# Kernel optimization log

Measured on AMD Instinct MI355X. Metric: run time of the kernel, lower is better.

Reference implementation:

```python
import jax, jax.numpy as jnp
import numpy as np

N = 50000      # nodes
E = 800000     # edges (avg degree 16)
D = 128        # node_embedding_dim
H = 256        # hidden_dim


def setup_inputs() -> dict:
    key = jax.random.key(0)
    ks = jax.random.split(key, 12)
    init = lambda k, shape, fan: (jax.random.normal(k, shape, jnp.float32) / np.sqrt(fan).astype(np.float32))
    return {
        "node_ids": jnp.arange(N, dtype=jnp.int32),
        "edge_index": jax.random.randint(ks[0], (2, E), 0, N, jnp.int32),
        "neighbour_edge_index": jax.random.randint(ks[1], (2, E), 0, N, jnp.int32),
        "edge_attr": jax.random.uniform(ks[2], (E,), jnp.float32),
        "emb": init(ks[3], (N, D), D),          # Embedding table
        "W_in": init(ks[4], (D, H), D), "b_in": jnp.zeros((H,), jnp.float32),
        "W_out": init(ks[5], (H, D), H), "b_out": jnp.zeros((D,), jnp.float32),
        "W1": init(ks[6], (2 * D, D), 2 * D), "b1": jnp.zeros((D,), jnp.float32),
        "W2": init(ks[7], (D, D), D), "b2": jnp.zeros((D,), jnp.float32),
        "W3": init(ks[8], (D, 1), D), "b3": jnp.zeros((1,), jnp.float32),
    }


def gcn_conv(x, W, b, edge_index, w):
    """PyG GCNConv, add_self_loops=False, normalize=True.
    out_i = b + sum_{(j->i)} d_i^{-1/2} w_ji d_j^{-1/2} (x_j @ W)
    deg_i = sum of incoming edge weights at target node i.
    """
    row, col = edge_index[0], edge_index[1]
    deg = jax.ops.segment_sum(w, col, num_segments=N)
    dinv = jnp.where(deg > 0, 1.0 / jnp.sqrt(deg), 0.0)
    norm = dinv[row] * w * dinv[col]                    # [E]
    h = x @ W                                           # [N, out]
    msg = h[row] * norm[:, None]                        # [E, out]
    return jax.ops.segment_sum(msg, col, num_segments=N) + b


def reference(node_ids, edge_index, neighbour_edge_index, edge_attr,
              emb, W_in, b_in, W_out, b_out, W1, b1, W2, b2, W3, b3):
    x = emb[node_ids]                                   # embedding lookup [N, D]
    x = jax.nn.elu(gcn_conv(x, W_in, b_in, edge_index, edge_attr))
    ones = jnp.ones((neighbour_edge_index.shape[1],), x.dtype)
    x = jax.nn.elu(gcn_conv(x, W_out, b_out, neighbour_edge_index, ones))
    # edge-level gather-concat-MLP decoder
    src, dst = edge_index[0], edge_index[1]
    h = jnp.concatenate([x[src], x[dst]], axis=1)       # [E, 2D]
    h = jax.nn.relu(h @ W1 + b1)
    h = jax.nn.relu(h @ W2 + b2)
    return (h @ W3 + b3).squeeze(-1)                    # [E]
```

## Files before the change

### kernel.cpp

```cpp
#include <hip/hip_runtime.h>
#include <math.h>

#define NN 50000
#define NE 800000

typedef __attribute__((ext_vector_type(8))) short s8_t;
typedef __attribute__((ext_vector_type(4))) float f4_t;

__device__ __forceinline__ short bf16_rne(float v) {
  unsigned u = __float_as_uint(v);
  unsigned r = (u + 0x7FFFu + ((u >> 16) & 1u)) >> 16;
  return (short)r;
}
__device__ __forceinline__ float bf16_tof(short h) {
  return __uint_as_float(((unsigned)(unsigned short)h) << 16);
}
__device__ __forceinline__ void split2(float v, short& hi, short& lo) {
  hi = bf16_rne(v);
  lo = bf16_rne(v - bf16_tof(hi));
}


__global__ __launch_bounds__(256) void k_wcvt(const float* __restrict__ W1,
                                              const float* __restrict__ W2,
                                              short* __restrict__ w1th,
                                              short* __restrict__ w1tl,
                                              short* __restrict__ w2th,
                                              short* __restrict__ w2tl) {
  int i = blockIdx.x * 256 + threadIdx.x;
  if (i < 32768) {
    int k = i >> 7, n = i & 127;
    short h, l; split2(W1[i], h, l);
    w1th[n * 256 + k] = h; w1tl[n * 256 + k] = l;
  } else if (i < 49152) {
    int j = i - 32768;
    int k = j >> 7, n = j & 127;
    short h, l; split2(W2[j], h, l);
    w2th[n * 128 + k] = h; w2tl[n * 128 + k] = l;
  }
}


__global__ __launch_bounds__(256) void k_hist(const int* __restrict__ ei,
                                              const int* __restrict__ nei,
                                              const float* __restrict__ w,
                                              int* __restrict__ cnt1,
                                              float* __restrict__ deg1,
                                              int* __restrict__ cnt2) {
  int e = blockIdx.x * 256 + threadIdx.x;
  if (e < NE) {
    int c1 = ei[NE + e];
    atomicAdd(&cnt1[c1], 1);
    atomicAdd(&deg1[c1], w[e]);
    atomicAdd(&cnt2[nei[NE + e]], 1);
  }
}

__global__ __launch_bounds__(256) void k_dinvs(const float* __restrict__ deg1,
                                               const int* __restrict__ cnt2,
                                               float* __restrict__ dinv1,
                                               float* __restrict__ dinv2) {
  int i = blockIdx.x * 256 + threadIdx.x;
  if (i < NN) {
    float d1 = deg1[i];
    dinv1[i] = d1 > 0.f ? (1.0f / sqrtf(d1)) : 0.f;
    int c2 = cnt2[i];
    dinv2[i] = c2 > 0 ? (1.0f / sqrtf((float)c2)) : 0.f;
  }
}


#define NCHUNK 196

__global__ __launch_bounds__(256) void k_scan_part(const int* __restrict__ cnt1,
                                                   const int* __restrict__ cnt2,
                                                   int* __restrict__ part) {
  int g = blockIdx.x >= NCHUNK;
  int chunk = g ? blockIdx.x - NCHUNK : blockIdx.x;
  const int* cnt = g ? cnt2 : cnt1;
  int i = chunk * 256 + threadIdx.x;
  int v = (i < NN) ? cnt[i] : 0;
  __shared__ int sd[4];
#pragma unroll
  for (int o = 32; o; o >>= 1) v += __shfl_down(v, o);
  if ((threadIdx.x & 63) == 0) sd[threadIdx.x >> 6] = v;
  __syncthreads();
  if (threadIdx.x == 0) part[blockIdx.x] = sd[0] + sd[1] + sd[2] + sd[3];
}

__global__ __launch_bounds__(256) void k_scan_mid(int* __restrict__ part,
                                                  int* __restrict__ off1_last,
                                                  int* __restrict__ off2_last) {
  __shared__ int sd[256];
  for (int g = 0; g < 2; g++) {
    int base = g * NCHUNK;
    int v = (threadIdx.x < NCHUNK) ? part[base + threadIdx.x] : 0;
    sd[threadIdx.x] = v;
    __syncthreads();
    for (int o = 1; o < 256; o <<= 1) {
      int x = (threadIdx.x >= o) ? sd[threadIdx.x - o] : 0;
      __syncthreads();
      sd[threadIdx.x] += x;
      __syncthreads();
    }
    if (threadIdx.x < NCHUNK) part[base + threadIdx.x] = sd[threadIdx.x] - v;
    if (threadIdx.x == 255) *(g ? off2_last : off1_last) = sd[255];
    __syncthreads();
  }
}

__global__ __launch_bounds__(256) void k_scan_final(const int* __restrict__ cnt1,
                                                    const int* __restrict__ cnt2,
                                                    const int* __restrict__ part,
                                                    int* __restrict__ off1,
                                                    int* __restrict__ pos1,
                                                    int* __restrict__ off2,
                                                    int* __restrict__ pos2) {
  int g = blockIdx.x >= NCHUNK;
  int chunk = g ? blockIdx.x - NCHUNK : blockIdx.x;
  const int* cnt = g ? cnt2 : cnt1;
  int* off = g ? off2 : off1;
  int* pos = g ? pos2 : pos1;
  __shared__ int sd[256];
  int i = chunk * 256 + threadIdx.x;
  int v = (i < NN) ? cnt[i] : 0;
  sd[threadIdx.x] = v;
  __syncthreads();
  for (int o = 1; o < 256; o <<= 1) {
    int x = (threadIdx.x >= o) ? sd[threadIdx.x - o] : 0;
    __syncthreads();
    sd[threadIdx.x] += x;
    __syncthreads();
  }
  if (i < NN) {
    int ex = part[blockIdx.x] + sd[threadIdx.x] - v;
    off[i] = ex; pos[i] = ex;
  }
}


__global__ __launch_bounds__(256) void k_fill(const int* __restrict__ ei,
                                              const int* __restrict__ nei,
                                              const float* __restrict__ w,
                                              const float* __restrict__ dinv1,
                                              const float* __restrict__ dinv2,
                                              int* __restrict__ pos1,
                                              int4* __restrict__ c1pack,
                                              int* __restrict__ pos2,
                                              int2* __restrict__ c2pack) {
  int e = blockIdx.x * 256 + threadIdx.x;
  if (e < NE) {
    int r = ei[e], c = ei[NE + e];
    float nv = dinv1[r] * w[e] * dinv1[c];
    int s = atomicAdd(&pos1[c], 1);
    c1pack[s] = make_int4(r, c, e, __float_as_int(nv));
    int r2 = nei[e], c2v = nei[NE + e];
    float nv2 = dinv2[r2] * dinv2[c2v];
    int s2 = atomicAdd(&pos2[c2v], 1);
    c2pack[s2] = make_int2(r2, __float_as_int(nv2));
  }
}


__global__ __launch_bounds__(256) void k_agg1(const int* __restrict__ off,
                                              const int4* __restrict__ c1pack,
                                              const int* __restrict__ ids,
                                              const float* __restrict__ emb,
                                              float* __restrict__ aggX) {
  int wave = threadIdx.x >> 6, lane = threadIdx.x & 63;
  int node = blockIdx.x * 4 + wave;
  int start = off[node], end = off[node + 1];
  float2 acc = make_float2(0.f, 0.f);
  int i = start;
  for (; i + 7 < end; i += 8) {
    float2 v[8]; float n[8];
#pragma unroll
    for (int k = 0; k < 8; k++) {
      int4 p = c1pack[i + k];
      n[k] = __int_as_float(p.w);
      v[k] = *(const float2*)(emb + (size_t)ids[p.x] * 128 + lane * 2);
    }
#pragma unroll
    for (int k = 0; k < 8; k++) {
      acc.x = fmaf(n[k], v[k].x, acc.x);
      acc.y = fmaf(n[k], v[k].y, acc.y);
    }
  }
  for (; i < end; i++) {
    int4 p = c1pack[i];
    float n0 = __int_as_float(p.w);
    float2 v0 = *(const float2*)(emb + (size_t)ids[p.x] * 128 + lane * 2);
    acc.x = fmaf(n0, v0.x, acc.x);
    acc.y = fmaf(n0, v0.y, acc.y);
  }
  *(float2*)(aggX + (size_t)node * 128 + lane * 2) = acc;
}


__global__ __launch_bounds__(256) void k_agg2(const int* __restrict__ off,
                                              const int2* __restrict__ c2pack,
                                              const float* __restrict__ h2,
                                              const float* __restrict__ b,
                                              short* __restrict__ xh,
                                              short* __restrict__ xl) {
  int wave = threadIdx.x >> 6, lane = threadIdx.x & 63;
  int node = blockIdx.x * 4 + wave;
  int start = off[node], end = off[node + 1];
  float2 acc = make_float2(0.f, 0.f);
  int i = start;
  for (; i + 7 < end; i += 8) {
    float2 v[8]; float n[8];
#pragma unroll
    for (int k = 0; k < 8; k++) {
      int2 p = c2pack[i + k];
      n[k] = __int_as_float(p.y);
      v[k] = *(const float2*)(h2 + (size_t)p.x * 128 + lane * 2);
    }
#pragma unroll
    for (int k = 0; k < 8; k++) {
      acc.x = fmaf(n[k], v[k].x, acc.x);
      acc.y = fmaf(n[k], v[k].y, acc.y);
    }
  }
  for (; i < end; i++) {
    int2 p = c2pack[i];
    float n0 = __int_as_float(p.y);
    float2 v0 = *(const float2*)(h2 + (size_t)p.x * 128 + lane * 2);
    acc.x = fmaf(n0, v0.x, acc.x);
    acc.y = fmaf(n0, v0.y, acc.y);
  }
  float vx = acc.x + b[lane * 2];
  float vy = acc.y + b[lane * 2 + 1];
  vx = vx > 0.f ? vx : expm1f(vx);
  vy = vy > 0.f ? vy : expm1f(vy);
  short hx, lx, hy, ly;
  split2(vx, hx, lx);
  split2(vy, hy, ly);
  unsigned hp = (unsigned)(unsigned short)hx | ((unsigned)(unsigned short)hy << 16);
  unsigned lp = (unsigned)(unsigned short)lx | ((unsigned)(unsigned short)ly << 16);
  *(unsigned*)(xh + (size_t)node * 128 + lane * 2) = hp;
  *(unsigned*)(xl + (size_t)node * 128 + lane * 2) = lp;
}


__global__ __launch_bounds__(256) void k_gemm_aggin(const float* __restrict__ X,
                                                    const float* __restrict__ W,
                                                    const float* __restrict__ b,
                                                    float* __restrict__ C) {
  __shared__ float As[32][128];
  int r0 = blockIdx.x * 32;
  int t = threadIdx.x;
  for (int i = t; i < 1024; i += 256) {
    int r = i >> 5, q = (i & 31) << 2;
    int rr = r0 + r;
    float4 v = make_float4(0.f, 0.f, 0.f, 0.f);
    if (rr < NN) v = *(const float4*)(X + (size_t)rr * 128 + q);
    *(float4*)(&As[r][q]) = v;
  }
  __syncthreads();
  int tc = t & 31, tr = t >> 5;
  int c0 = tc * 8, rr0 = tr * 4;
  float acc[4][8];
#pragma unroll
  for (int r = 0; r < 4; r++)
#pragma unroll
    for (int c = 0; c < 8; c++) acc[r][c] = 0.f;

  for (int k0 = 0; k0 < 128; k0 += 4) {
    float a_[4][4];
#pragma unroll
    for (int r = 0; r < 4; r++) {
      float4 v = *(const float4*)(&As[rr0 + r][k0]);
      a_[r][0] = v.x; a_[r][1] = v.y; a_[r][2] = v.z; a_[r][3] = v.w;
    }
#pragma unroll
    for (int kk = 0; kk < 4; kk++) {
      float4 w0 = *(const float4*)(W + (size_t)(k0 + kk) * 256 + c0);
      float4 w1 = *(const float4*)(W + (size_t)(k0 + kk) * 256 + c0 + 4);
#pragma unroll
      for (int r = 0; r < 4; r++) {
        float av = a_[r][kk];
        acc[r][0] += av * w0.x; acc[r][1] += av * w0.y;
        acc[r][2] += av * w0.z; acc[r][3] += av * w0.w;
        acc[r][4] += av * w1.x; acc[r][5] += av * w1.y;
        acc[r][6] += av * w1.z; acc[r][7] += av * w1.w;
      }
    }
  }
  float4 bb0 = *(const float4*)(b + c0);
  float4 bb1 = *(const float4*)(b + c0 + 4);
#pragma unroll
  for (int r = 0; r < 4; r++) {
    int rr = r0 + rr0 + r;
    if (rr < NN) {
      float o[8];
      o[0] = acc[r][0] + bb0.x; o[1] = acc[r][1] + bb0.y;
      o[2] = acc[r][2] + bb0.z; o[3] = acc[r][3] + bb0.w;
      o[4] = acc[r][4] + bb1.x; o[5] = acc[r][5] + bb1.y;
      o[6] = acc[r][6] + bb1.z; o[7] = acc[r][7] + bb1.w;
#pragma unroll
      for (int c = 0; c < 8; c++) o[c] = o[c] > 0.f ? o[c] : expm1f(o[c]);
      *(float4*)(C + (size_t)rr * 256 + c0) = make_float4(o[0], o[1], o[2], o[3]);
      *(float4*)(C + (size_t)rr * 256 + c0 + 4) = make_float4(o[4], o[5], o[6], o[7]);
    }
  }
}


__global__ __launch_bounds__(256) void k_gemm_mid(const float* __restrict__ X,
                                                  const float* __restrict__ W,
                                                  float* __restrict__ C) {
  __shared__ float As[32][256];
  int r0 = blockIdx.x * 32;
  int t = threadIdx.x;
  for (int i = t; i < 2048; i += 256) {
    int r = i >> 6, q = (i & 63) << 2;
    int rr = r0 + r;
    float4 v = make_float4(0.f, 0.f, 0.f, 0.f);
    if (rr < NN) v = *(const float4*)(X + (size_t)rr * 256 + q);
    *(float4*)(&As[r][q]) = v;
  }
  __syncthreads();
  int tc = t & 31, tr = t >> 5;
  int c0 = tc * 4, rr0 = tr * 4;
  float acc[4][4];
#pragma unroll
  for (int r = 0; r < 4; r++)
#pragma unroll
    for (int c = 0; c < 4; c++) acc[r][c] = 0.f;

  for (int k0 = 0; k0 < 256; k0 += 4) {
    float a_[4][4];
#pragma unroll
    for (int r = 0; r < 4; r++) {
      float4 v = *(const float4*)(&As[rr0 + r][k0]);
      a_[r][0] = v.x; a_[r][1] = v.y; a_[r][2] = v.z; a_[r][3] = v.w;
    }
#pragma unroll
    for (int kk = 0; kk < 4; kk++) {
      float4 w = *(const float4*)(W + (size_t)(k0 + kk) * 128 + c0);
#pragma unroll
      for (int r = 0; r < 4; r++) {
        float av = a_[r][kk];
        acc[r][0] += av * w.x; acc[r][1] += av * w.y;
        acc[r][2] += av * w.z; acc[r][3] += av * w.w;
      }
    }
  }
#pragma unroll
  for (int r = 0; r < 4; r++) {
    int rr = r0 + rr0 + r;
    if (rr < NN) {
      float4 o = make_float4(acc[r][0], acc[r][1], acc[r][2], acc[r][3]);
      *(float4*)(C + (size_t)rr * 128 + c0) = o;
    }
  }
}


__global__ __launch_bounds__(256) void k_pab(const short* __restrict__ x2h,
                                             const short* __restrict__ x2l,
                                             const short* __restrict__ w1th,
                                             const short* __restrict__ w1tl,
                                             const float* __restrict__ b1,
                                             float* __restrict__ Pa,
                                             float* __restrict__ Pb) {
  __shared__ short Xh[32 * 136];
  __shared__ short Xl[32 * 136];
  int t = threadIdx.x;
  int n0 = blockIdx.x * 32;
#pragma unroll
  for (int j = 0; j < 2; j++) {
    int i = t + 256 * j;
    int row = i >> 4, q = i & 15;
    int node = n0 + row; if (node >= NN) node = NN - 1;
    *(uint4*)&Xh[row * 136 + q * 8] = *(const uint4*)(x2h + (size_t)node * 128 + q * 8);
    *(uint4*)&Xl[row * 136 + q * 8] = *(const uint4*)(x2l + (size_t)node * 128 + q * 8);
  }
  __syncthreads();

  int w = t >> 6, lane = t & 63;
  int quad = lane >> 4, l16 = lane & 15;
  int nb = w * 32;
  int aoff0 = l16 * 136 + quad * 8;
  int aoff1 = (16 + l16) * 136 + quad * 8;
  int bo0 = (nb + l16) * 256 + quad * 8;
  int bo1 = (nb + 16 + l16) * 256 + quad * 8;

  f4_t aa[2][2], ab[2][2];
#pragma unroll
  for (int mi = 0; mi < 2; mi++)
#pragma unroll
    for (int ni = 0; ni < 2; ni++) {
      aa[mi][ni] = (f4_t){0.f, 0.f, 0.f, 0.f};
      ab[mi][ni] = (f4_t){0.f, 0.f, 0.f, 0.f};
    }

#pragma unroll
  for (int kb = 0; kb < 4; kb++) {
    int k0 = kb * 32;
    s8_t ah0 = *(const s8_t*)&Xh[aoff0 + k0];
    s8_t ah1 = *(const s8_t*)&Xh[aoff1 + k0];
    s8_t al0 = *(const s8_t*)&Xl[aoff0 + k0];
    s8_t al1 = *(const s8_t*)&Xl[aoff1 + k0];
    {
      s8_t bh0 = *(const s8_t*)(w1th + bo0 + k0);
      s8_t bh1 = *(const s8_t*)(w1th + bo1 + k0);
      s8_t bl0 = *(const s8_t*)(w1tl + bo0 + k0);
      s8_t bl1 = *(const s8_t*)(w1tl + bo1 + k0);
      aa[0][0] = __builtin_amdgcn_mfma_f32_16x16x32_bf16(ah0, bh0, aa[0][0], 0, 0, 0);
      aa[0][0] = __builtin_amdgcn_mfma_f32_16x16x32_bf16(ah0, bl0, aa[0][0], 0, 0, 0);
      aa[0][0] = __builtin_amdgcn_mfma_f32_16x16x32_bf16(al0, bh0, aa[0][0], 0, 0, 0);
      aa[0][1] = __builtin_amdgcn_mfma_f32_16x16x32_bf16(ah0, bh1, aa[0][1], 0, 0, 0);
      aa[0][1] = __builtin_amdgcn_mfma_f32_16x16x32_bf16(ah0, bl1, aa[0][1], 0, 0, 0);
      aa[0][1] = __builtin_amdgcn_mfma_f32_16x16x32_bf16(al0, bh1, aa[0][1], 0, 0, 0);
      aa[1][0] = __builtin_amdgcn_mfma_f32_16x16x32_bf16(ah1, bh0, aa[1][0], 0, 0, 0);
      aa[1][0] = __builtin_amdgcn_mfma_f32_16x16x32_bf16(ah1, bl0, aa[1][0], 0, 0, 0);
      aa[1][0] = __builtin_amdgcn_mfma_f32_16x16x32_bf16(al1, bh0, aa[1][0], 0, 0, 0);
      aa[1][1] = __builtin_amdgcn_mfma_f32_16x16x32_bf16(ah1, bh1, aa[1][1], 0, 0, 0);
      aa[1][1] = __builtin_amdgcn_mfma_f32_16x16x32_bf16(ah1, bl1, aa[1][1], 0, 0, 0);
      aa[1][1] = __builtin_amdgcn_mfma_f32_16x16x32_bf16(al1, bh1, aa[1][1], 0, 0, 0);
    }
    {
      s8_t bh0 = *(const s8_t*)(w1th + bo0 + 128 + k0);
      s8_t bh1 = *(const s8_t*)(w1th + bo1 + 128 + k0);
      s8_t bl0 = *(const s8_t*)(w1tl + bo0 + 128 + k0);
      s8_t bl1 = *(const s8_t*)(w1tl + bo1 + 128 + k0);
      ab[0][0] = __builtin_amdgcn_mfma_f32_16x16x32_bf16(ah0, bh0, ab[0][0], 0, 0, 0);
      ab[0][0] = __builtin_amdgcn_mfma_f32_16x16x32_bf16(ah0, bl0, ab[0][0], 0, 0, 0);
      ab[0][0] = __builtin_amdgcn_mfma_f32_16x16x32_bf16(al0, bh0, ab[0][0], 0, 0, 0);
      ab[0][1] = __builtin_amdgcn_mfma_f32_16x16x32_bf16(ah0, bh1, ab[0][1], 0, 0, 0);
      ab[0][1] = __builtin_amdgcn_mfma_f32_16x16x32_bf16(ah0, bl1, ab[0][1], 0, 0, 0);
      ab[0][1] = __builtin_amdgcn_mfma_f32_16x16x32_bf16(al0, bh1, ab[0][1], 0, 0, 0);
      ab[1][0] = __builtin_amdgcn_mfma_f32_16x16x32_bf16(ah1, bh0, ab[1][0], 0, 0, 0);
      ab[1][0] = __builtin_amdgcn_mfma_f32_16x16x32_bf16(ah1, bl0, ab[1][0], 0, 0, 0);
      ab[1][0] = __builtin_amdgcn_mfma_f32_16x16x32_bf16(al1, bh0, ab[1][0], 0, 0, 0);
      ab[1][1] = __builtin_amdgcn_mfma_f32_16x16x32_bf16(ah1, bh1, ab[1][1], 0, 0, 0);
      ab[1][1] = __builtin_amdgcn_mfma_f32_16x16x32_bf16(ah1, bl1, ab[1][1], 0, 0, 0);
      ab[1][1] = __builtin_amdgcn_mfma_f32_16x16x32_bf16(al1, bh1, ab[1][1], 0, 0, 0);
    }
  }

  float b1v0 = b1[nb + l16], b1v1 = b1[nb + 16 + l16];
#pragma unroll
  for (int mi = 0; mi < 2; mi++)
#pragma unroll
    for (int ni = 0; ni < 2; ni++) {
      int col = nb + ni * 16 + l16;
      float bv = ni ? b1v1 : b1v0;
#pragma unroll
      for (int r = 0; r < 4; r++) {
        int node = n0 + mi * 16 + quad * 4 + r;
        if (node < NN) {
          Pa[(size_t)node * 128 + col] = aa[mi][ni][r];
          Pb[(size_t)node * 128 + col] = ab[mi][ni][r] + bv;
        }
      }
    }
}


#define ST 136

__global__ __launch_bounds__(256, 4) void k_decoder(
    const float* __restrict__ Pa, const float* __restrict__ Pb,
    const int4* __restrict__ c1pack,
    const short* __restrict__ w2th, const short* __restrict__ w2tl,
    const float* __restrict__ b2,
    const float* __restrict__ W3, const float* __restrict__ b3,
    float* __restrict__ out) {
  __shared__ short Th[32 * ST];
  __shared__ short Tl[32 * ST];
  __shared__ float part[4][32];

  int t = threadIdx.x;
  int b = blockIdx.x;
  int id = (b & 7) * 3125 + (b >> 3);
  int s0base = id * 32;

#pragma unroll
  for (int j = 0; j < 2; j++) {
    int i = t + 256 * j;
    int le = i >> 4, q = i & 15;
    int4 p = c1pack[s0base + le];
    const float* pa = Pa + (size_t)p.x * 128 + q * 8;
    const float* pb = Pb + (size_t)p.y * 128 + q * 8;
    float4 a0 = *(const float4*)(pa);
    float4 a1 = *(const float4*)(pa + 4);
    float4 c0 = *(const float4*)(pb);
    float4 c1 = *(const float4*)(pb + 4);
    float v[8];
    v[0] = a0.x + c0.x; v[1] = a0.y + c0.y;
    v[2] = a0.z + c0.z; v[3] = a0.w + c0.w;
    v[4] = a1.x + c1.x; v[5] = a1.y + c1.y;
    v[6] = a1.z + c1.z; v[7] = a1.w + c1.w;
    s8_t hv, lv;
#pragma unroll
    for (int k = 0; k < 8; k++) {
      float x = fmaxf(v[k], 0.f);
      short h, l; split2(x, h, l);
      hv[k] = h; lv[k] = l;
    }
    *(s8_t*)&Th[le * ST + q * 8] = hv;
    *(s8_t*)&Tl[le * ST + q * 8] = lv;
  }
  __syncthreads();

  int w = t >> 6, lane = t & 63;
  int quad = lane >> 4, l16 = lane & 15;
  int nb = w * 32;
  float b2v0 = b2[nb + l16], b2v1 = b2[nb + 16 + l16];
  float w3a = W3[nb + l16], w3b = W3[nb + 16 + l16];

  int toff0 = l16 * ST + quad * 8;
  int toff1 = (16 + l16) * ST + quad * 8;
  int coff0 = (nb + l16) * 128 + quad * 8;
  int coff1 = (nb + 16 + l16) * 128 + quad * 8;

  f4_t acc2[2][2];
#pragma unroll
  for (int mi = 0; mi < 2; mi++)
#pragma unroll
    for (int ni = 0; ni < 2; ni++) acc2[mi][ni] = (f4_t){0.f, 0.f, 0.f, 0.f};

#pragma unroll
  for (int kb = 0; kb < 4; kb++) {
    int k0 = kb * 32;
    s8_t ah0 = *(const s8_t*)&Th[toff0 + k0];
    s8_t ah1 = *(const s8_t*)&Th[toff1 + k0];
    s8_t al0 = *(const s8_t*)&Tl[toff0 + k0];
    s8_t al1 = *(const s8_t*)&Tl[toff1 + k0];
    s8_t bh0 = *(const s8_t*)(w2th + coff0 + k0);
    s8_t bh1 = *(const s8_t*)(w2th + coff1 + k0);
    s8_t bl0 = *(const s8_t*)(w2tl + coff0 + k0);
    s8_t bl1 = *(const s8_t*)(w2tl + coff1 + k0);
    acc2[0][0] = __builtin_amdgcn_mfma_f32_16x16x32_bf16(ah0, bh0, acc2[0][0], 0, 0, 0);
    acc2[0][0] = __builtin_amdgcn_mfma_f32_16x16x32_bf16(ah0, bl0, acc2[0][0], 0, 0, 0);
    acc2[0][0] = __builtin_amdgcn_mfma_f32_16x16x32_bf16(al0, bh0, acc2[0][0], 0, 0, 0);
    acc2[0][1] = __builtin_amdgcn_mfma_f32_16x16x32_bf16(ah0, bh1, acc2[0][1], 0, 0, 0);
    acc2[0][1] = __builtin_amdgcn_mfma_f32_16x16x32_bf16(ah0, bl1, acc2[0][1], 0, 0, 0);
    acc2[0][1] = __builtin_amdgcn_mfma_f32_16x16x32_bf16(al0, bh1, acc2[0][1], 0, 0, 0);
    acc2[1][0] = __builtin_amdgcn_mfma_f32_16x16x32_bf16(ah1, bh0, acc2[1][0], 0, 0, 0);
    acc2[1][0] = __builtin_amdgcn_mfma_f32_16x16x32_bf16(ah1, bl0, acc2[1][0], 0, 0, 0);
    acc2[1][0] = __builtin_amdgcn_mfma_f32_16x16x32_bf16(al1, bh0, acc2[1][0], 0, 0, 0);
    acc2[1][1] = __builtin_amdgcn_mfma_f32_16x16x32_bf16(ah1, bh1, acc2[1][1], 0, 0, 0);
    acc2[1][1] = __builtin_amdgcn_mfma_f32_16x16x32_bf16(ah1, bl1, acc2[1][1], 0, 0, 0);
    acc2[1][1] = __builtin_amdgcn_mfma_f32_16x16x32_bf16(al1, bh1, acc2[1][1], 0, 0, 0);
  }

#pragma unroll
  for (int mi = 0; mi < 2; mi++) {
#pragma unroll
    for (int r = 0; r < 4; r++) {
      float pv = fmaxf(acc2[mi][0][r] + b2v0, 0.f) * w3a +
                 fmaxf(acc2[mi][1][r] + b2v1, 0.f) * w3b;
      pv += __shfl_xor(pv, 1);
      pv += __shfl_xor(pv, 2);
      pv += __shfl_xor(pv, 4);
      pv += __shfl_xor(pv, 8);
      if (l16 == 0) part[w][mi * 16 + quad * 4 + r] = pv;
    }
  }
  __syncthreads();

  if (t < 32) {
    float s = part[0][t] + part[1][t] + part[2][t] + part[3][t] + b3[0];
    int4 p = c1pack[s0base + t];
    out[p.z] = s;
  }
}


extern "C" void kernel_launch(void* const* d_in, const int* in_sizes, int n_in,
                              void* d_out, int out_size, void* d_ws, size_t ws_size,
                              hipStream_t stream) {
  const int*   node_ids = (const int*)d_in[0];
  const int*   ei       = (const int*)d_in[1];
  const int*   nei      = (const int*)d_in[2];
  const float* eattr    = (const float*)d_in[3];
  const float* emb      = (const float*)d_in[4];
  const float* W_in     = (const float*)d_in[5];
  const float* b_in     = (const float*)d_in[6];
  const float* W_out    = (const float*)d_in[7];
  const float* b_out    = (const float*)d_in[8];
  const float* W1       = (const float*)d_in[9];
  const float* b1       = (const float*)d_in[10];
  const float* W2       = (const float*)d_in[11];
  const float* b2       = (const float*)d_in[12];
  const float* W3       = (const float*)d_in[13];
  const float* b3       = (const float*)d_in[14];
  float* out = (float*)d_out;

  float* ws    = (float*)d_ws;
  float* bufA  = ws;
  float* bufB  = bufA + (size_t)NN * 128;
  int*   cnt1  = (int*)(bufB + (size_t)NN * 256);
  int*   cnt2  = cnt1 + NN;
  float* deg1  = (float*)(cnt2 + NN);
  float* dinv1 = deg1 + NN;
  float* dinv2 = dinv1 + NN;
  int*   off1  = (int*)(dinv2 + NN);
  int*   pos1  = off1 + NN + 1;
  int*   off2  = pos1 + NN;
  int*   pos2  = off2 + NN + 1;
  int4*  c1pack = (int4*)((((uintptr_t)(pos2 + NN)) + 15) & ~(uintptr_t)15);
  int2*  c2pack = (int2*)(c1pack + NE);
  short* w1th  = (short*)(c2pack + NE);
  short* w1tl  = w1th + 32768;
  short* w2th  = w1tl + 32768;
  short* w2tl  = w2th + 16384;
  int*   part  = (int*)(w2tl + 16384);

  float* aggX  = bufA;
  float* h2    = bufA;
  float* Pa    = bufA;
  float* x1    = bufB;
  short* x2h   = (short*)bufB;
  short* x2l   = x2h + (size_t)NN * 128;
  float* Pb    = bufB + (size_t)NN * 128;

  k_wcvt<<<192, 256, 0, stream>>>(W1, W2, w1th, w1tl, w2th, w2tl);

  hipMemsetAsync(cnt1, 0, 3 * (size_t)NN * sizeof(int), stream);
  k_hist<<<NE / 256, 256, 0, stream>>>(ei, nei, eattr, cnt1, deg1, cnt2);
  k_dinvs<<<(NN + 255) / 256, 256, 0, stream>>>(deg1, cnt2, dinv1, dinv2);
  k_scan_part<<<2 * NCHUNK, 256, 0, stream>>>(cnt1, cnt2, part);
  k_scan_mid<<<1, 256, 0, stream>>>(part, off1 + NN, off2 + NN);
  k_scan_final<<<2 * NCHUNK, 256, 0, stream>>>(cnt1, cnt2, part,
                                               off1, pos1, off2, pos2);
  k_fill<<<NE / 256, 256, 0, stream>>>(ei, nei, eattr, dinv1, dinv2,
                                       pos1, c1pack, pos2, c2pack);

  k_agg1<<<NN / 4, 256, 0, stream>>>(off1, c1pack, node_ids, emb, aggX);
  k_gemm_aggin<<<(NN + 31) / 32, 256, 0, stream>>>(aggX, W_in, b_in, x1);

  k_gemm_mid<<<(NN + 31) / 32, 256, 0, stream>>>(x1, W_out, h2);
  k_agg2<<<NN / 4, 256, 0, stream>>>(off2, c2pack, h2, b_out, x2h, x2l);

  k_pab<<<(NN + 31) / 32, 256, 0, stream>>>(x2h, x2l, w1th, w1tl, b1, Pa, Pb);

  k_decoder<<<NE / 32, 256, 0, stream>>>(Pa, Pb, c1pack,
                                         w2th, w2tl, b2, W3, b3, out);
}
```

Before: 806.6 us.

## Move node GEMMs to split-bf16 MFMA and widen aggregation gathers to float4

The two node-level GEMMs (X·W_in and x1·W_out), which used scalar FP32 FMA, now run on bf16 MFMA. Each operand is split into hi/lo bf16 halves and three products are accumulated, approximating FP32 accuracy. W_in and W_out are pre-transposed and split in the weight-conversion kernel, and activations are written as hi/lo bf16 pairs. The aggregation kernels now let each half-wave handle alternate edges with float4 loads, then combine the halves with a cross-lane shuffle. This adds conversion work and drops the lo*lo term, so results carry a small precision risk.

New measurement: 760.7 us. 1.06x faster.

```diff
diff --git a/kernel.cpp b/kernel.cpp
--- a/kernel.cpp
+++ b/kernel.cpp
@@ -23,10 +23,16 @@
 
 __global__ __launch_bounds__(256) void k_wcvt(const float* __restrict__ W1,
                                               const float* __restrict__ W2,
+                                              const float* __restrict__ W_in,
+                                              const float* __restrict__ W_out,
                                               short* __restrict__ w1th,
                                               short* __restrict__ w1tl,
                                               short* __restrict__ w2th,
-                                              short* __restrict__ w2tl) {
+                                              short* __restrict__ w2tl,
+                                              short* __restrict__ winth,
+                                              short* __restrict__ wintl,
+                                              short* __restrict__ woutth,
+                                              short* __restrict__ wouttl) {
   int i = blockIdx.x * 256 + threadIdx.x;
   if (i < 32768) {
     int k = i >> 7, n = i & 127;
@@ -37,6 +43,16 @@
     int k = j >> 7, n = j & 127;
     short h, l; split2(W2[j], h, l);
     w2th[n * 128 + k] = h; w2tl[n * 128 + k] = l;
+  } else if (i < 81920) {
+    int j = i - 49152;
+    int k = j >> 8, n = j & 255;
+    short h, l; split2(W_in[j], h, l);
+    winth[n * 128 + k] = h; wintl[n * 128 + k] = l;
+  } else if (i < 114688) {
+    int j = i - 81920;
+    int k = j >> 7, n = j & 127;
+    short h, l; split2(W_out[j], h, l);
+    woutth[n * 256 + k] = h; wouttl[n * 256 + k] = l;
   }
 }
 
@@ -166,34 +182,55 @@
                                               const int4* __restrict__ c1pack,
                                               const int* __restrict__ ids,
                                               const float* __restrict__ emb,
-                                              float* __restrict__ aggX) {
+                                              short* __restrict__ aggXh,
+                                              short* __restrict__ aggXl) {
   int wave = threadIdx.x >> 6, lane = threadIdx.x & 63;
+  int h = lane >> 5, sub = lane & 31;
   int node = blockIdx.x * 4 + wave;
   int start = off[node], end = off[node + 1];
-  float2 acc = make_float2(0.f, 0.f);
-  int i = start;
-  for (; i + 7 < end; i += 8) {
-    float2 v[8]; float n[8];
+  float4 acc = make_float4(0.f, 0.f, 0.f, 0.f);
+  int i = start + h;
+  for (; i + 14 < end; i += 16) {
+    float4 v[8]; float n[8];
 #pragma unroll
     for (int k = 0; k < 8; k++) {
-      int4 p = c1pack[i + k];
+      int4 p = c1pack[i + 2 * k];
       n[k] = __int_as_float(p.w);
-      v[k] = *(const float2*)(emb + (size_t)ids[p.x] * 128 + lane * 2);
+      v[k] = *(const float4*)(emb + (size_t)ids[p.x] * 128 + sub * 4);
     }
 #pragma unroll
     for (int k = 0; k < 8; k++) {
       acc.x = fmaf(n[k], v[k].x, acc.x);
       acc.y = fmaf(n[k], v[k].y, acc.y);
-    }
-  }
-  for (; i < end; i++) {
+      acc.z = fmaf(n[k], v[k].z, acc.z);
+      acc.w = fmaf(n[k], v[k].w, acc.w);
+    }
+  }
+  for (; i < end; i += 2) {
     int4 p = c1pack[i];
     float n0 = __int_as_float(p.w);
-    float2 v0 = *(const float2*)(emb + (size_t)ids[p.x] * 128 + lane * 2);
+    float4 v0 = *(const float4*)(emb + (size_t)ids[p.x] * 128 + sub * 4);
     acc.x = fmaf(n0, v0.x, acc.x);
     acc.y = fmaf(n0, v0.y, acc.y);
-  }
-  *(float2*)(aggX + (size_t)node * 128 + lane * 2) = acc;
+    acc.z = fmaf(n0, v0.z, acc.z);
+    acc.w = fmaf(n0, v0.w, acc.w);
+  }
+  acc.x += __shfl_xor(acc.x, 32);
+  acc.y += __shfl_xor(acc.y, 32);
+  acc.z += __shfl_xor(acc.z, 32);
+  acc.w += __shfl_xor(acc.w, 32);
+  if (h == 0) {
+    short h0, l0, h1, l1, h2, l2, h3, l3;
+    split2(acc.x, h0, l0); split2(acc.y, h1, l1);
+    split2(acc.z, h2, l2); split2(acc.w, h3, l3);
+    uint2 hp, lp;
+    hp.x = (unsigned)(unsigned short)h0 | ((unsigned)(unsigned short)h1 << 16);
+    hp.y = (unsigned)(unsigned short)h2 | ((unsigned)(unsigned short)h3 << 16);
+    lp.x = (unsigned)(unsigned short)l0 | ((unsigned)(unsigned short)l1 << 16);
+    lp.y = (unsigned)(unsigned short)l2 | ((unsigned)(unsigned short)l3 << 16);
+    *(uint2*)(aggXh + (size_t)node * 128 + sub * 4) = hp;
+    *(uint2*)(aggXl + (size_t)node * 128 + sub * 4) = lp;
+  }
 }
 
 
@@ -204,157 +241,200 @@
                                               short* __restrict__ xh,
                                               short* __restrict__ xl) {
   int wave = threadIdx.x >> 6, lane = threadIdx.x & 63;
+  int h = lane >> 5, sub = lane & 31;
   int node = blockIdx.x * 4 + wave;
   int start = off[node], end = off[node + 1];
-  float2 acc = make_float2(0.f, 0.f);
-  int i = start;
-  for (; i + 7 < end; i += 8) {
-    float2 v[8]; float n[8];
+  float4 acc = make_float4(0.f, 0.f, 0.f, 0.f);
+  int i = start + h;
+  for (; i + 14 < end; i += 16) {
+    float4 v[8]; float n[8];
 #pragma unroll
     for (int k = 0; k < 8; k++) {
-      int2 p = c2pack[i + k];
+      int2 p = c2pack[i + 2 * k];
       n[k] = __int_as_float(p.y);
-      v[k] = *(const float2*)(h2 + (size_t)p.x * 128 + lane * 2);
+      v[k] = *(const float4*)(h2 + (size_t)p.x * 128 + sub * 4);
     }
 #pragma unroll
     for (int k = 0; k < 8; k++) {
       acc.x = fmaf(n[k], v[k].x, acc.x);
       acc.y = fmaf(n[k], v[k].y, acc.y);
-    }
-  }
-  for (; i < end; i++) {
+      acc.z = fmaf(n[k], v[k].z, acc.z);
+      acc.w = fmaf(n[k], v[k].w, acc.w);
+    }
+  }
+  for (; i < end; i += 2) {
     int2 p = c2pack[i];
     float n0 = __int_as_float(p.y);
-    float2 v0 = *(const float2*)(h2 + (size_t)p.x * 128 + lane * 2);
+    float4 v0 = *(const float4*)(h2 + (size_t)p.x * 128 + sub * 4);
     acc.x = fmaf(n0, v0.x, acc.x);
     acc.y = fmaf(n0, v0.y, acc.y);
-  }
-  float vx = acc.x + b[lane * 2];
-  float vy = acc.y + b[lane * 2 + 1];
-  vx = vx > 0.f ? vx : expm1f(vx);
-  vy = vy > 0.f ? vy : expm1f(vy);
-  short hx, lx, hy, ly;
-  split2(vx, hx, lx);
-  split2(vy, hy, ly);
-  unsigned hp = (unsigned)(unsigned short)hx | ((unsigned)(unsigned short)hy << 16);
-  unsigned lp = (unsigned)(unsigned short)lx | ((unsigned)(unsigned short)ly << 16);
-  *(unsigned*)(xh + (size_t)node * 128 + lane * 2) = hp;
-  *(unsigned*)(xl + (size_t)node * 128 + lane * 2) = lp;
-}
-
-
-__global__ __launch_bounds__(256) void k_gemm_aggin(const float* __restrict__ X,
-                                                    const float* __restrict__ W,
-                                                    const float* __restrict__ b,
-                                                    float* __restrict__ C) {
-  __shared__ float As[32][128];
-  int r0 = blockIdx.x * 32;
+    acc.z = fmaf(n0, v0.z, acc.z);
+    acc.w = fmaf(n0, v0.w, acc.w);
+  }
+  acc.x += __shfl_xor(acc.x, 32);
+  acc.y += __shfl_xor(acc.y, 32);
+  acc.z += __shfl_xor(acc.z, 32);
+  acc.w += __shfl_xor(acc.w, 32);
+  if (h == 0) {
+    float4 bb = *(const float4*)(b + sub * 4);
+    float v0 = acc.x + bb.x, v1 = acc.y + bb.y;
+    float v2 = acc.z + bb.z, v3 = acc.w + bb.w;
+    v0 = v0 > 0.f ? v0 : expm1f(v0);
+    v1 = v1 > 0.f ? v1 : expm1f(v1);
+    v2 = v2 > 0.f ? v2 : expm1f(v2);
+    v3 = v3 > 0.f ? v3 : expm1f(v3);
+    short h0, l0, h1, l1, h2s, l2, h3, l3;
+    split2(v0, h0, l0); split2(v1, h1, l1);
+    split2(v2, h2s, l2); split2(v3, h3, l3);
+    uint2 hp, lp;
+    hp.x = (unsigned)(unsigned short)h0 | ((unsigned)(unsigned short)h1 << 16);
+    hp.y = (unsigned)(unsigned short)h2s | ((unsigned)(unsigned short)h3 << 16);
+    lp.x = (unsigned)(unsigned short)l0 | ((unsigned)(unsigned short)l1 << 16);
+    lp.y = (unsigned)(unsigned short)l2 | ((unsigned)(unsigned short)l3 << 16);
+    *(uint2*)(xh + (size_t)node * 128 + sub * 4) = hp;
+    *(uint2*)(xl + (size_t)node * 128 + sub * 4) = lp;
+  }
+}
+
+
+__global__ __launch_bounds__(256) void k_gemm1m(const short* __restrict__ aggXh,
+                                                const short* __restrict__ aggXl,
+                                                const short* __restrict__ winth,
+                                                const short* __restrict__ wintl,
+                                                const float* __restrict__ b,
+                                                short* __restrict__ x1h,
+                                                short* __restrict__ x1l) {
+  __shared__ short Xh[32 * 136];
+  __shared__ short Xl[32 * 136];
   int t = threadIdx.x;
-  for (int i = t; i < 1024; i += 256) {
-    int r = i >> 5, q = (i & 31) << 2;
-    int rr = r0 + r;
-    float4 v = make_float4(0.f, 0.f, 0.f, 0.f);
-    if (rr < NN) v = *(const float4*)(X + (size_t)rr * 128 + q);
-    *(float4*)(&As[r][q]) = v;
+  int n0 = blockIdx.x * 32;
+#pragma unroll
+  for (int j = 0; j < 2; j++) {
+    int i = t + 256 * j;
+    int row = i >> 4, q = i & 15;
+    int node = n0 + row; if (node >= NN) node = NN - 1;
+    *(uint4*)&Xh[row * 136 + q * 8] = *(const uint4*)(aggXh + (size_t)node * 128 + q * 8);
+    *(uint4*)&Xl[row * 136 + q * 8] = *(const uint4*)(aggXl + (size_t)node * 128 + q * 8);
   }
   __syncthreads();
-  int tc = t & 31, tr = t >> 5;
-  int c0 = tc * 8, rr0 = tr * 4;
-  float acc[4][8];
-#pragma unroll
-  for (int r = 0; r < 4; r++)
-#pragma unroll
-    for (int c = 0; c < 8; c++) acc[r][c] = 0.f;
-
-  for (int k0 = 0; k0 < 128; k0 += 4) {
-    float a_[4][4];
-#pragma unroll
-    for (int r = 0; r < 4; r++) {
-      float4 v = *(const float4*)(&As[rr0 + r][k0]);
-      a_[r][0] = v.x; a_[r][1] = v.y; a_[r][2] = v.z; a_[r][3] = v.w;
-    }
-#pragma unroll
-    for (int kk = 0; kk < 4; kk++) {
-      float4 w0 = *(const float4*)(W + (size_t)(k0 + kk) * 256 + c0);
-      float4 w1 = *(const float4*)(W + (size_t)(k0 + kk) * 256 + c0 + 4);
+
+  int w = t >> 6, lane = t & 63;
+  int quad = lane >> 4, l16 = lane & 15;
+  int nb = w * 64;
+  int aoff0 = l16 * 136 + quad * 8;
+  int aoff1 = (16 + l16) * 136 + quad * 8;
+
+  f4_t acc[2][4];
+#pragma unroll
+  for (int mi = 0; mi < 2; mi++)
+#pragma unroll
+    for (int ni = 0; ni < 4; ni++) acc[mi][ni] = (f4_t){0.f, 0.f, 0.f, 0.f};
+
+#pragma unroll
+  for (int kb = 0; kb < 4; kb++) {
+    int k0 = kb * 32;
+    s8_t ah0 = *(const s8_t*)&Xh[aoff0 + k0];
+    s8_t ah1 = *(const s8_t*)&Xh[aoff1 + k0];
+    s8_t al0 = *(const s8_t*)&Xl[aoff0 + k0];
+    s8_t al1 = *(const s8_t*)&Xl[aoff1 + k0];
+#pragma unroll
+    for (int ni = 0; ni < 4; ni++) {
+      int bo = (nb + ni * 16 + l16) * 128 + quad * 8 + k0;
+      s8_t bh = *(const s8_t*)(winth + bo);
+      s8_t bl = *(const s8_t*)(wintl + bo);
+      acc[0][ni] = __builtin_amdgcn_mfma_f32_16x16x32_bf16(ah0, bh, acc[0][ni], 0, 0, 0);
+      acc[0][ni] = __builtin_amdgcn_mfma_f32_16x16x32_bf16(ah0, bl, acc[0][ni], 0, 0, 0);
+      acc[0][ni] = __builtin_amdgcn_mfma_f32_16x16x32_bf16(al0, bh, acc[0][ni], 0, 0, 0);
+      acc[1][ni] = __builtin_amdgcn_mfma_f32_16x16x32_bf16(ah1, bh, acc[1][ni], 0, 0, 0);
+      acc[1][ni] = __builtin_amdgcn_mfma_f32_16x16x32_bf16(ah1, bl, acc[1][ni], 0, 0, 0);
+      acc[1][ni] = __builtin_amdgcn_mfma_f32_16x16x32_bf16(al1, bh, acc[1][ni], 0, 0, 0);
+    }
+  }
+
+#pragma unroll
+  for (int mi = 0; mi < 2; mi++)
+#pragma unroll
+    for (int ni = 0; ni < 4; ni++) {
+      int col = nb + ni * 16 + l16;
+      float bv = b[col];
 #pragma unroll
       for (int r = 0; r < 4; r++) {
-        float av = a_[r][kk];
-        acc[r][0] += av * w0.x; acc[r][1] += av * w0.y;
-        acc[r][2] += av * w0.z; acc[r][3] += av * w0.w;
-        acc[r][4] += av * w1.x; acc[r][5] += av * w1.y;
-        acc[r][6] += av * w1.z; acc[r][7] += av * w1.w;
+        int node = n0 + mi * 16 + quad * 4 + r;
+        if (node < NN) {
+          float v = acc[mi][ni][r] + bv;
+          v = v > 0.f ? v : expm1f(v);
+          short hh, ll; split2(v, hh, ll);
+          x1h[(size_t)node * 256 + col] = hh;
+          x1l[(size_t)node * 256 + col] = ll;
+        }
       }
     }
-  }
-  float4 bb0 = *(const float4*)(b + c0);
-  float4 bb1 = *(const float4*)(b + c0 + 4);
-#pragma unroll
-  for (int r = 0; r < 4; r++) {
-    int rr = r0 + rr0 + r;
-    if (rr < NN) {
-      float o[8];
-      o[0] = acc[r][0] + bb0.x; o[1] = acc[r][1] + bb0.y;
-      o[2] = acc[r][2] + bb0.z; o[3] = acc[r][3] + bb0.w;
-      o[4] = acc[r][4] + bb1.x; o[5] = acc[r][5] + bb1.y;
-      o[6] = acc[r][6] + bb1.z; o[7] = acc[r][7] + bb1.w;
-#pragma unroll
-      for (int c = 0; c < 8; c++) o[c] = o[c] > 0.f ? o[c] : expm1f(o[c]);
-      *(float4*)(C + (size_t)rr * 256 + c0) = make_float4(o[0], o[1], o[2], o[3]);
-      *(float4*)(C + (size_t)rr * 256 + c0 + 4) = make_float4(o[4], o[5], o[6], o[7]);
-    }
-  }
-}
-
-
-__global__ __launch_bounds__(256) void k_gemm_mid(const float* __restrict__ X,
-                                                  const float* __restrict__ W,
-                                                  float* __restrict__ C) {
-  __shared__ float As[32][256];
-  int r0 = blockIdx.x * 32;
+}
+
+
+__global__ __launch_bounds__(256) void k_gemm2m(const short* __restrict__ x1h,
+                                                const short* __restrict__ x1l,
+                                                const short* __restrict__ woutth,
+                                                const short* __restrict__ wouttl,
+                                                float* __restrict__ h2) {
+  __shared__ short Xh[32 * 264];
+  __shared__ short Xl[32 * 264];
   int t = threadIdx.x;
-  for (int i = t; i < 2048; i += 256) {
-    int r = i >> 6, q = (i & 63) << 2;
-    int rr = r0 + r;
-    float4 v = make_float4(0.f, 0.f, 0.f, 0.f);
-    if (rr < NN) v = *(const float4*)(X + (size_t)rr * 256 + q);
-    *(float4*)(&As[r][q]) = v;
+  int n0 = blockIdx.x * 32;
+#pragma unroll
+  for (int j = 0; j < 4; j++) {
+    int i = t + 256 * j;
+    int row = i >> 5, q = i & 31;
+    int node = n0 + row; if (node >= NN) node = NN - 1;
+    *(uint4*)&Xh[row * 264 + q * 8] = *(const uint4*)(x1h + (size_t)node * 256 + q * 8);
+    *(uint4*)&Xl[row * 264 + q * 8] = *(const uint4*)(x1l + (size_t)node * 256 + q * 8);
   }
   __syncthreads();
-  int tc = t & 31, tr = t >> 5;
-  int c0 = tc * 4, rr0 = tr * 4;
-  float acc[4][4];
-#pragma unroll
-  for (int r = 0; r < 4; r++)
-#pragma unroll
-    for (int c = 0; c < 4; c++) acc[r][c] = 0.f;
-
-  for (int k0 = 0; k0 < 256; k0 += 4) {
-    float a_[4][4];
-#pragma unroll
-    for (int r = 0; r < 4; r++) {
-      float4 v = *(const float4*)(&As[rr0 + r][k0]);
-      a_[r][0] = v.x; a_[r][1] = v.y; a_[r][2] = v.z; a_[r][3] = v.w;
-    }
-#pragma unroll
-    for (int kk = 0; kk < 4; kk++) {
-      float4 w = *(const float4*)(W + (size_t)(k0 + kk) * 128 + c0);
+
+  int w = t >> 6, lane = t & 63;
+  int quad = lane >> 4, l16 = lane & 15;
+  int nb = w * 32;
+  int aoff0 = l16 * 264 + quad * 8;
+  int aoff1 = (16 + l16) * 264 + quad * 8;
+
+  f4_t acc[2][2];
+#pragma unroll
+  for (int mi = 0; mi < 2; mi++)
+#pragma unroll
+    for (int ni = 0; ni < 2; ni++) acc[mi][ni] = (f4_t){0.f, 0.f, 0.f, 0.f};
+
+#pragma unroll
+  for (int kb = 0; kb < 8; kb++) {
+    int k0 = kb * 32;
+    s8_t ah0 = *(const s8_t*)&Xh[aoff0 + k0];
+    s8_t ah1 = *(const s8_t*)&Xh[aoff1 + k0];
+    s8_t al0 = *(const s8_t*)&Xl[aoff0 + k0];
+    s8_t al1 = *(const s8_t*)&Xl[aoff1 + k0];
+#pragma unroll
+    for (int ni = 0; ni < 2; ni++) {
+      int bo = (nb + ni * 16 + l16) * 256 + quad * 8 + k0;
+      s8_t bh = *(const s8_t*)(woutth + bo);
+      s8_t bl = *(const s8_t*)(wouttl + bo);
+      acc[0][ni] = __builtin_amdgcn_mfma_f32_16x16x32_bf16(ah0, bh, acc[0][ni], 0, 0, 0);
+      acc[0][ni] = __builtin_amdgcn_mfma_f32_16x16x32_bf16(ah0, bl, acc[0][ni], 0, 0, 0);
+      acc[0][ni] = __builtin_amdgcn_mfma_f32_16x16x32_bf16(al0, bh, acc[0][ni], 0, 0, 0);
+      acc[1][ni] = __builtin_amdgcn_mfma_f32_16x16x32_bf16(ah1, bh, acc[1][ni], 0, 0, 0);
+      acc[1][ni] = __builtin_amdgcn_mfma_f32_16x16x32_bf16(ah1, bl, acc[1][ni], 0, 0, 0);
+      acc[1][ni] = __builtin_amdgcn_mfma_f32_16x16x32_bf16(al1, bh, acc[1][ni], 0, 0, 0);
+    }
+  }
+
+#pragma unroll
+  for (int mi = 0; mi < 2; mi++)
+#pragma unroll
+    for (int ni = 0; ni < 2; ni++) {
+      int col = nb + ni * 16 + l16;
 #pragma unroll
       for (int r = 0; r < 4; r++) {
-        float av = a_[r][kk];
-        acc[r][0] += av * w.x; acc[r][1] += av * w.y;
-        acc[r][2] += av * w.z; acc[r][3] += av * w.w;
+        int node = n0 + mi * 16 + quad * 4 + r;
+        if (node < NN) h2[(size_t)node * 128 + col] = acc[mi][ni][r];
       }
     }
-  }
-#pragma unroll
-  for (int r = 0; r < 4; r++) {
-    int rr = r0 + rr0 + r;
-    if (rr < NN) {
-      float4 o = make_float4(acc[r][0], acc[r][1], acc[r][2], acc[r][3]);
-      *(float4*)(C + (size_t)rr * 128 + c0) = o;
-    }
-  }
 }
 
 
@@ -605,21 +685,29 @@
   int*   pos2  = off2 + NN + 1;
   int4*  c1pack = (int4*)((((uintptr_t)(pos2 + NN)) + 15) & ~(uintptr_t)15);
   int2*  c2pack = (int2*)(c1pack + NE);
-  short* w1th  = (short*)(c2pack + NE);
-  short* w1tl  = w1th + 32768;
-  short* w2th  = w1tl + 32768;
-  short* w2tl  = w2th + 16384;
-  int*   part  = (int*)(w2tl + 16384);
-
-  float* aggX  = bufA;
+  short* w1th   = (short*)(c2pack + NE);
+  short* w1tl   = w1th + 32768;
+  short* w2th   = w1tl + 32768;
+  short* w2tl   = w2th + 16384;
+  short* winth  = w2tl + 16384;
+  short* wintl  = winth + 32768;
+  short* woutth = wintl + 32768;
+  short* wouttl = woutth + 32768;
+  int*   part   = (int*)(wouttl + 32768);
+
+  short* aggXh = (short*)bufA;
+  short* aggXl = aggXh + (size_t)NN * 128;
   float* h2    = bufA;
   float* Pa    = bufA;
-  float* x1    = bufB;
+  short* x1h   = (short*)bufB;
+  short* x1l   = x1h + (size_t)NN * 256;
   short* x2h   = (short*)bufB;
   short* x2l   = x2h + (size_t)NN * 128;
   float* Pb    = bufB + (size_t)NN * 128;
 
-  k_wcvt<<<192, 256, 0, stream>>>(W1, W2, w1th, w1tl, w2th, w2tl);
+  k_wcvt<<<448, 256, 0, stream>>>(W1, W2, W_in, W_out,
+                                  w1th, w1tl, w2th, w2tl,
+                                  winth, wintl, woutth, wouttl);
 
   hipMemsetAsync(cnt1, 0, 3 * (size_t)NN * sizeof(int), stream);
   k_hist<<<NE / 256, 256, 0, stream>>>(ei, nei, eattr, cnt1, deg1, cnt2);
@@ -631,10 +719,11 @@
   k_fill<<<NE / 256, 256, 0, stream>>>(ei, nei, eattr, dinv1, dinv2,
                                        pos1, c1pack, pos2, c2pack);
 
-  k_agg1<<<NN / 4, 256, 0, stream>>>(off1, c1pack, node_ids, emb, aggX);
-  k_gemm_aggin<<<(NN + 31) / 32, 256, 0, stream>>>(aggX, W_in, b_in, x1);
-
-  k_gemm_mid<<<(NN + 31) / 32, 256, 0, stream>>>(x1, W_out, h2);
+  k_agg1<<<NN / 4, 256, 0, stream>>>(off1, c1pack, node_ids, emb, aggXh, aggXl);
+  k_gemm1m<<<(NN + 31) / 32, 256, 0, stream>>>(aggXh, aggXl, winth, wintl,
+                                               b_in, x1h, x1l);
+
+  k_gemm2m<<<(NN + 31) / 32, 256, 0, stream>>>(x1h, x1l, woutth, wouttl, h2);
   k_agg2<<<NN / 4, 256, 0, stream>>>(off2, c2pack, h2, b_out, x2h, x2l);
 
   k_pab<<<(NN + 31) / 32, 256, 0, stream>>>(x2h, x2l, w1th, w1tl, b1, Pa, Pb);
```
